# Kernel tuning notes

Measured on AMD Instinct MI355X. Metric: run time of the kernel, lower is better.

## Reference

```python
import jax, jax.numpy as jnp
import numpy as np

B, N, C = 2, 2048, 1024
H = 16
D = C // H
HID = 4 * C
EPS = 1e-5


def layernorm(x, g, b):
    mu = jnp.mean(x, axis=-1, keepdims=True)
    var = jnp.var(x, axis=-1, keepdims=True)
    return (x - mu) * jax.lax.rsqrt(var + EPS) * g + b


def setup_inputs() -> dict:
    key = jax.random.key(0)
    ks = jax.random.split(key, 8)
    s = lambda fan_in: 1.0 / np.sqrt(fan_in)
    return {
        "x": jax.random.normal(ks[0], (B, N, C), dtype=jnp.float32),
        "ln1_g": jnp.ones((C,), jnp.float32),
        "ln1_b": jnp.zeros((C,), jnp.float32),
        "w_qkv": jax.random.normal(ks[1], (C, 3 * C), jnp.float32) * s(C),
        "w_proj": jax.random.normal(ks[2], (C, C), jnp.float32) * s(C),
        "b_proj": jnp.zeros((C,), jnp.float32),
        "ln2_g": jnp.ones((C,), jnp.float32),
        "ln2_b": jnp.zeros((C,), jnp.float32),
        "w_fc1": jax.random.normal(ks[3], (C, HID), jnp.float32) * s(C),
        "b_fc1": jnp.zeros((HID,), jnp.float32),
        "w_fc2": jax.random.normal(ks[4], (HID, C), jnp.float32) * s(HID),
        "b_fc2": jnp.zeros((C,), jnp.float32),
        "metadata": 0,
        "thw_shape": 2048,
    }


def reference(x, ln1_g, ln1_b, w_qkv, w_proj, b_proj, ln2_g, ln2_b,
              w_fc1, b_fc1, w_fc2, b_fc2, metadata, thw_shape):
    scale = 1.0 / np.sqrt(D)
    # --- attention branch (pre-norm) ---
    xn = layernorm(x, ln1_g, ln1_b)
    qkv = (xn @ w_qkv).reshape(B, N, 3, H, D)
    q = jnp.transpose(qkv[:, :, 0], (0, 2, 1, 3))  # [B,H,N,D]
    k = jnp.transpose(qkv[:, :, 1], (0, 2, 1, 3))
    v = jnp.transpose(qkv[:, :, 2], (0, 2, 1, 3))
    attn = jax.nn.softmax(jnp.einsum('bhnd,bhmd->bhnm', q, k) * scale, axis=-1)
    o = jnp.einsum('bhnm,bhmd->bhnd', attn, v)
    o = jnp.transpose(o, (0, 2, 1, 3)).reshape(B, N, C)
    x = x + (o @ w_proj + b_proj)
    # --- MLP branch (pre-norm) ---
    xn2 = layernorm(x, ln2_g, ln2_b)
    h = jax.nn.gelu(xn2 @ w_fc1 + b_fc1, approximate=False)  # torch GELU = exact erf
    x = x + (h @ w_fc2 + b_fc2)
    return x
```

## Files before the change

### kernel.cpp

```cpp
#include <hip/hip_runtime.h>

#define B_   2
#define N_   2048
#define C_   1024
#define H_   16
#define D_   64
#define HID_ 4096
#define M_   (B_ * N_)

typedef __attribute__((ext_vector_type(8))) short bf16x8;
typedef __attribute__((ext_vector_type(4))) float f32x4;

__device__ __forceinline__ unsigned short f2bf(float f) {
  unsigned int u = __builtin_bit_cast(unsigned int, f);
  u += 0x7fffu + ((u >> 16) & 1u);
  return (unsigned short)(u >> 16);
}

__device__ __forceinline__ unsigned int cvtpk(float a, float b) {
  unsigned int r;
  asm("v_cvt_pk_bf16_f32 %0, %1, %2" : "=v"(r) : "v"(a), "v"(b));
  return r;
}

__device__ __forceinline__ float exp2a(float x) {
  float r;
  asm("v_exp_f32 %0, %1" : "=v"(r) : "v"(x));
  return r;
}

__device__ __forceinline__ void gl2lds16(const void* g, void* l) {
  __builtin_amdgcn_global_load_lds(
      (const __attribute__((address_space(1))) unsigned int*)g,
      (__attribute__((address_space(3))) unsigned int*)l, 16, 0, 0);
}

#define LOG2E 1.44269504088896f

__global__ __launch_bounds__(256) void ln_kernel(const float* __restrict__ x,
                                                 const float* __restrict__ g,
                                                 const float* __restrict__ bta,
                                                 unsigned short* __restrict__ out) {
  int row  = blockIdx.x * 4 + (threadIdx.x >> 6);
  int lane = threadIdx.x & 63;
  const float* xr = x + (size_t)row * C_;
  float4 v[4];
  float s1 = 0.f, s2 = 0.f;
#pragma unroll
  for (int j = 0; j < 4; j++) {
    v[j] = *(const float4*)(xr + j * 256 + lane * 4);
    s1 += v[j].x + v[j].y + v[j].z + v[j].w;
    s2 += v[j].x * v[j].x + v[j].y * v[j].y + v[j].z * v[j].z + v[j].w * v[j].w;
  }
#pragma unroll
  for (int m = 1; m < 64; m <<= 1) { s1 += __shfl_xor(s1, m); s2 += __shfl_xor(s2, m); }
  float mu  = s1 * (1.0f / C_);
  float var = s2 * (1.0f / C_) - mu * mu;
  float rs  = rsqrtf(var + 1e-5f);
#pragma unroll
  for (int j = 0; j < 4; j++) {
    const float4 gv = *(const float4*)(g + j * 256 + lane * 4);
    const float4 bv = *(const float4*)(bta + j * 256 + lane * 4);
    ushort4 o;
    o.x = f2bf((v[j].x - mu) * rs * gv.x + bv.x);
    o.y = f2bf((v[j].y - mu) * rs * gv.y + bv.y);
    o.z = f2bf((v[j].z - mu) * rs * gv.z + bv.z);
    o.w = f2bf((v[j].w - mu) * rs * gv.w + bv.w);
    *(ushort4*)(out + (size_t)row * C_ + j * 256 + lane * 4) = o;
  }
}

__global__ __launch_bounds__(256) void wtrans_all(
    const float* __restrict__ w0, const float* __restrict__ w1,
    const float* __restrict__ w2, const float* __restrict__ w3,
    unsigned short* __restrict__ o0, unsigned short* __restrict__ o1,
    unsigned short* __restrict__ o2, unsigned short* __restrict__ o3) {
  int id = blockIdx.x;
  const float* W; unsigned short* Wt; int K, N, rel;
  if (id < 3072)      { W = w0; Wt = o0; K = 1024; N = 3072; rel = id; }
  else if (id < 4096) { W = w1; Wt = o1; K = 1024; N = 1024; rel = id - 3072; }
  else if (id < 8192) { W = w2; Wt = o2; K = 1024; N = 4096; rel = id - 4096; }
  else                { W = w3; Wt = o3; K = 4096; N = 1024; rel = id - 8192; }
  int nx = N >> 5;
  int n0 = (rel % nx) * 32, k0 = (rel / nx) * 32;
  __shared__ float t[32][33];
  int tx = threadIdx.x, ty = threadIdx.y;
#pragma unroll
  for (int j = 0; j < 4; j++)
    t[ty + j * 8][tx] = W[(size_t)(k0 + ty + j * 8) * N + n0 + tx];
  __syncthreads();
#pragma unroll
  for (int j = 0; j < 4; j++)
    Wt[(size_t)(n0 + ty + j * 8) * K + k0 + tx] = f2bf(t[tx][ty + j * 8]);
}

__global__ __launch_bounds__(256) void gemm_db_kernel(
    const unsigned short* __restrict__ A,
    const unsigned short* __restrict__ Wt,
    const float* __restrict__ bias,
    const float* __restrict__ resid,
    float* __restrict__ outf,
    int M, int N, int K) {
  __shared__ __align__(16) short As[2][128][64];
  __shared__ __align__(16) short Bs[2][64][64];
  int tid = threadIdx.x;
  int w = tid >> 6, lane = tid & 63, r = lane & 15, quad = lane >> 4;
  int rowbase = w * 32;

  int nwg = gridDim.x * gridDim.y;
  int lin = blockIdx.y * gridDim.x + blockIdx.x;
  int cpx = nwg >> 3;
  lin = (lin & 7) * cpx + (lin >> 3);
  int bx = lin % gridDim.x, by = lin / gridDim.x;
  int bM = by * 128, bN = bx * 64;

  int srow   = (w << 3) + (lane >> 3);
  int schunk = (lane & 7) ^ ((lane >> 3) & 7);
  const unsigned short* aP = A  + (size_t)(bM + srow) * K + schunk * 8;
  const unsigned short* bP = Wt + (size_t)(bN + srow) * K + schunk * 8;

  int pc0 = (quad ^ (r & 7)) * 8;

  f32x4 acc[2][4];
#pragma unroll
  for (int i = 0; i < 2; i++)
#pragma unroll
    for (int j = 0; j < 4; j++) acc[i][j] = f32x4{0.f, 0.f, 0.f, 0.f};

#define STAGE_DB(kt, b)                                                       \
  do {                                                                        \
    int k0_ = (kt) * 64;                                                      \
    _Pragma("unroll") for (int p = 0; p < 4; p++)                             \
      gl2lds16(aP + (size_t)(p * 32) * K + k0_, &As[b][p * 32 + (w << 3)][0]);\
    _Pragma("unroll") for (int p = 0; p < 2; p++)                             \
      gl2lds16(bP + (size_t)(p * 32) * K + k0_, &Bs[b][p * 32 + (w << 3)][0]);\
  } while (0)

  const int nk = K >> 6;
  STAGE_DB(0, 0);
  __syncthreads();

  for (int kt = 0; kt < nk; kt++) {
    const int cb = kt & 1;
    if (kt + 1 < nk) STAGE_DB(kt + 1, cb ^ 1);
#pragma unroll
    for (int kh = 0; kh < 2; kh++) {
      int pc = pc0 ^ (kh * 32);
      bf16x8 af[2], bfr[4];
#pragma unroll
      for (int mt = 0; mt < 2; mt++)
        af[mt] = *(const bf16x8*)&As[cb][rowbase + mt * 16 + r][pc];
#pragma unroll
      for (int nt = 0; nt < 4; nt++)
        bfr[nt] = *(const bf16x8*)&Bs[cb][nt * 16 + r][pc];
#pragma unroll
      for (int mt = 0; mt < 2; mt++)
#pragma unroll
        for (int nt = 0; nt < 4; nt++)
          acc[mt][nt] = __builtin_amdgcn_mfma_f32_16x16x32_bf16(af[mt], bfr[nt], acc[mt][nt], 0, 0, 0);
    }
    __syncthreads();
  }

#pragma unroll
  for (int mt = 0; mt < 2; mt++) {
#pragma unroll
    for (int nt = 0; nt < 4; nt++) {
#pragma unroll
      for (int i = 0; i < 4; i++) {
        int gm = bM + rowbase + mt * 16 + quad * 4 + i;
        int gn = bN + nt * 16 + r;
        outf[(size_t)gm * N + gn] = acc[mt][nt][i] + bias[gn] + resid[(size_t)gm * N + gn];
      }
    }
  }
#undef STAGE_DB
}

template <int MODE>
__global__ __launch_bounds__(512, 2) void gemm256_kernel(
    const unsigned short* __restrict__ A,
    const unsigned short* __restrict__ Wt,
    const float* __restrict__ bias,
    unsigned short* __restrict__ outb0,
    unsigned short* __restrict__ outb1,
    unsigned short* __restrict__ outb2,
    int M, int N, int K) {
  __shared__ __align__(16) short As[2][256][64];
  __shared__ __align__(16) short Bs[2][256][64];
  const int tid = threadIdx.x;
  const int w = tid >> 6, lane = tid & 63, r = lane & 15, quad = lane >> 4;
  const int wr = w >> 2, wc = w & 3;

  int nwg = gridDim.x * gridDim.y;
  int lin = blockIdx.y * gridDim.x + blockIdx.x;
  int cpx = nwg >> 3;
  lin = (lin & 7) * cpx + (lin >> 3);
  const int bN = (lin % gridDim.x) * 256, bM = (lin / gridDim.x) * 256;

  const int srow   = (w << 3) + (lane >> 3);
  const int schunk = (lane & 7) ^ ((lane >> 3) & 7);
  const unsigned short* aSrc = A  + (size_t)(bM + srow) * K + schunk * 8;
  const unsigned short* bSrc = Wt + (size_t)(bN + srow) * K + schunk * 8;
  const int wrow = w << 3;

  const int ntiles = K >> 6;
  const int tmask  = ntiles - 1;

#define STAGE_H(t, h)                                                            \
  do {                                                                           \
    int b_ = (t) & 1, tt_ = (t) & tmask;                                         \
    if ((h) < 2) {                                                               \
      const unsigned short* p_ = aSrc + (size_t)((h) * 128) * K + tt_ * 64;      \
      gl2lds16(p_, &As[b_][(h) * 128 + wrow][0]);                                \
      gl2lds16(p_ + (size_t)64 * K, &As[b_][(h) * 128 + 64 + wrow][0]);          \
    } else {                                                                     \
      const unsigned short* p_ = bSrc + (size_t)(((h) - 2) * 128) * K + tt_ * 64;\
      gl2lds16(p_, &Bs[b_][((h) - 2) * 128 + wrow][0]);                          \
      gl2lds16(p_ + (size_t)64 * K, &Bs[b_][((h) - 2) * 128 + 64 + wrow][0]);    \
    }                                                                            \
  } while (0)

  f32x4 acc[8][4];
#pragma unroll
  for (int i = 0; i < 8; i++)
#pragma unroll
    for (int j = 0; j < 4; j++) acc[i][j] = f32x4{0.f, 0.f, 0.f, 0.f};

  bf16x8 af[4][2];
  bf16x8 bfr[4][2];

#define RD_A(b, msub)                                                            \
  {                                                                              \
    _Pragma("unroll") for (int mt_ = 0; mt_ < 4; mt_++)                          \
      _Pragma("unroll") for (int ks_ = 0; ks_ < 2; ks_++)                        \
        af[mt_][ks_] = *(const bf16x8*)&As[b][wr * 128 + (msub) * 64 + mt_ * 16 + r] \
                                          [((ks_ * 4 + quad) ^ (r & 7)) * 8];    \
  }
#define RD_B(b, nh)                                                              \
  {                                                                              \
    _Pragma("unroll") for (int nt_ = 0; nt_ < 2; nt_++)                          \
      _Pragma("unroll") for (int ks_ = 0; ks_ < 2; ks_++)                        \
        bfr[(nh) * 2 + nt_][ks_] =                                               \
            *(const bf16x8*)&Bs[b][wc * 64 + (nh) * 32 + nt_ * 16 + r]           \
                               [((ks_ * 4 + quad) ^ (r & 7)) * 8];               \
  }
#define MM_Q(msub, nh)                                                           \
  {                                                                              \
    _Pragma("unroll") for (int mt_ = 0; mt_ < 4; mt_++)                          \
      _Pragma("unroll") for (int nt_ = 0; nt_ < 2; nt_++)                        \
        _Pragma("unroll") for (int ks_ = 0; ks_ < 2; ks_++)                      \
          acc[(msub) * 4 + mt_][(nh) * 2 + nt_] =                                \
              __builtin_amdgcn_mfma_f32_16x16x32_bf16(                           \
                  af[mt_][ks_], bfr[(nh) * 2 + nt_][ks_],                        \
                  acc[(msub) * 4 + mt_][(nh) * 2 + nt_], 0, 0, 0);               \
  }

#define BARRIER() asm volatile("s_barrier" ::: "memory")
#define WAITL()   asm volatile("s_waitcnt lgkmcnt(0)" ::: "memory")
#define WAITV6()  asm volatile("s_waitcnt vmcnt(6)" ::: "memory")
#define PRIO1()   __builtin_amdgcn_s_setprio(1)
#define PRIO0()   __builtin_amdgcn_s_setprio(0)

  STAGE_H(0, 0); STAGE_H(0, 1); STAGE_H(0, 2); STAGE_H(0, 3);
  STAGE_H(1, 2); STAGE_H(1, 3); STAGE_H(1, 0);
  WAITV6();
  BARRIER();

  const int niter = ntiles >> 1;
  for (int i = 0; i < niter; i++) {
    const int tc = 2 * i;
    RD_A(0, 0); RD_B(0, 0);
    STAGE_H(tc + 1, 1);
    BARRIER(); WAITL();
    PRIO1(); MM_Q(0, 0); PRIO0();
    BARRIER();
    RD_B(0, 1);
    BARRIER(); WAITL();
    PRIO1(); MM_Q(0, 1); PRIO0();
    BARRIER();
    RD_A(0, 1);
    STAGE_H(tc + 2, 2);
    BARRIER(); WAITL();
    PRIO1(); MM_Q(1, 1); PRIO0();
    BARRIER();
    STAGE_H(tc + 2, 3); STAGE_H(tc + 2, 0);
    BARRIER(); WAITL();
    PRIO1(); MM_Q(1, 0); PRIO0();
    WAITV6();
    BARRIER();
    RD_A(1, 0); RD_B(1, 0);
    STAGE_H(tc + 2, 1);
    BARRIER(); WAITL();
    PRIO1(); MM_Q(0, 0); PRIO0();
    BARRIER();
    RD_B(1, 1);
    BARRIER(); WAITL();
    PRIO1(); MM_Q(0, 1); PRIO0();
    BARRIER();
    RD_A(1, 1);
    STAGE_H(tc + 3, 2);
    BARRIER(); WAITL();
    PRIO1(); MM_Q(1, 1); PRIO0();
    BARRIER();
    STAGE_H(tc + 3, 3); STAGE_H(tc + 3, 0);
    BARRIER(); WAITL();
    PRIO1(); MM_Q(1, 0); PRIO0();
    WAITV6();
    BARRIER();
  }

#pragma unroll
  for (int m = 0; m < 8; m++) {
#pragma unroll
    for (int n = 0; n < 4; n++) {
      int gm0 = bM + wr * 128 + m * 16 + quad * 4;
      int gn  = bN + wc * 64 + n * 16 + r;
      if (MODE == 0) {
        int s = gn >> 10, c = gn & 1023;
        int hh = c >> 6, d = c & 63;
        int b = gm0 >> 11, n0 = gm0 & 2047;
        if (s == 2) {
          unsigned int p0 = cvtpk(acc[m][n][0], acc[m][n][1]);
          unsigned int p1 = cvtpk(acc[m][n][2], acc[m][n][3]);
          *(uint2*)(outb2 + ((size_t)(b * H_ + hh) * D_ + d) * N_ + n0) = uint2{p0, p1};
        } else {
          unsigned short* dst = (s == 0) ? outb0 : outb1;
          float sc = (s == 0) ? 0.125f * LOG2E : 1.0f;
#pragma unroll
          for (int i2 = 0; i2 < 4; i2++) {
            size_t di = ((size_t)(b * H_ + hh) * N_ + n0 + i2) * D_ + d;
            dst[di] = f2bf(acc[m][n][i2] * sc);
          }
        }
      } else {
#pragma unroll
        for (int i2 = 0; i2 < 4; i2++) {
          float t = acc[m][n][i2] + bias[gn];
          float gl = 0.5f * t * (1.0f + erff(t * 0.70710678118f));
          outb0[(size_t)(gm0 + i2) * N + gn] = f2bf(gl);
        }
      }
    }
  }
#undef STAGE_H
#undef RD_A
#undef RD_B
#undef MM_Q
#undef BARRIER
#undef WAITL
#undef WAITV6
#undef PRIO1
#undef PRIO0
}

__global__ __launch_bounds__(512, 2) void attn_kernel(const unsigned short* __restrict__ qb,
                                                      const unsigned short* __restrict__ kb,
                                                      const unsigned short* __restrict__ vtb,
                                                      unsigned short* __restrict__ ob) {
  __shared__ __align__(16) short Ks[2][128][64];
  __shared__ __align__(16) short Vts[2][64][128];
  __shared__ __align__(16) short Pl[8 * 16 * 128];
  int tid = threadIdx.x;
  int w = tid >> 6, lane = tid & 63, r = lane & 15, quad = lane >> 4;
  int bh = blockIdx.x & 31, qt = blockIdx.x >> 5;
  const unsigned short* qh  = qb  + (size_t)bh * N_ * D_;
  const unsigned short* kh  = kb  + (size_t)bh * N_ * D_;
  const unsigned short* vth = vtb + (size_t)bh * D_ * N_;
  int swz = r & 7;

  bf16x8 qf[2][2];
#pragma unroll
  for (int mt = 0; mt < 2; mt++)
#pragma unroll
    for (int ks = 0; ks < 2; ks++)
      qf[mt][ks] = *(const bf16x8*)(qh + (size_t)(qt * 256 + w * 32 + mt * 16 + r) * D_ + ks * 32 + quad * 8);

  float mst[2] = {-1e30f, -1e30f}, lst[2] = {0.f, 0.f};
  f32x4 oacc[2][4];
#pragma unroll
  for (int mt = 0; mt < 2; mt++)
#pragma unroll
    for (int nt = 0; nt < 4; nt++) oacc[mt][nt] = f32x4{0.f, 0.f, 0.f, 0.f};

  const unsigned short* kBase = kh + (size_t)(tid >> 3) * D_ + ((tid & 7) ^ ((tid >> 3) & 7)) * 8;
  const unsigned short* vBase = vth + (size_t)(tid >> 4) * N_ + ((tid & 15) ^ ((tid >> 4) & 7)) * 8;

  short* Plw = &Pl[0] + w * 2048;

  gl2lds16(kBase,                        &Ks[0][(w << 3)][0]);
  gl2lds16(kBase + (size_t)64 * D_,      &Ks[0][64 + (w << 3)][0]);
  gl2lds16(vBase,                        &Vts[0][(w << 2)][0]);
  gl2lds16(vBase + (size_t)32 * N_,      &Vts[0][32 + (w << 2)][0]);
  __syncthreads();

  for (int t = 0; t < 16; t++) {
    const int cur = t & 1;
    if (t < 15) {
      const int nb = cur ^ 1;
      gl2lds16(kBase + (size_t)(t + 1) * 128 * D_,                  &Ks[nb][(w << 3)][0]);
      gl2lds16(kBase + (size_t)((t + 1) * 128 + 64) * D_,           &Ks[nb][64 + (w << 3)][0]);
      gl2lds16(vBase + (size_t)(t + 1) * 128,                       &Vts[nb][(w << 2)][0]);
      gl2lds16(vBase + (size_t)(t + 1) * 128 + (size_t)32 * N_,     &Vts[nb][32 + (w << 2)][0]);
    }

    f32x4 sacc[2][8];
#pragma unroll
    for (int mt = 0; mt < 2; mt++)
#pragma unroll
      for (int nt = 0; nt < 8; nt++) sacc[mt][nt] = f32x4{0.f, 0.f, 0.f, 0.f};
#pragma unroll
    for (int ks = 0; ks < 2; ks++) {
#pragma unroll
      for (int nt = 0; nt < 8; nt++) {
        bf16x8 kfr = *(const bf16x8*)&Ks[cur][nt * 16 + r][((ks * 4 + quad) ^ swz) * 8];
#pragma unroll
        for (int mt = 0; mt < 2; mt++)
          sacc[mt][nt] = __builtin_amdgcn_mfma_f32_16x16x32_bf16(kfr, qf[mt][ks], sacc[mt][nt], 0, 0, 0);
      }
    }

    bf16x8 vfr[4][4];
#pragma unroll
    for (int ks = 0; ks < 4; ks++)
#pragma unroll
      for (int nt2 = 0; nt2 < 4; nt2++)
        vfr[ks][nt2] = *(const bf16x8*)&Vts[cur][nt2 * 16 + r][((ks * 4 + quad) ^ swz) * 8];

#pragma unroll
    for (int mt = 0; mt < 2; mt++) {
      float tm = -1e30f;
#pragma unroll
      for (int nt = 0; nt < 8; nt++)
#pragma unroll
        for (int i = 0; i < 4; i++) tm = fmaxf(tm, sacc[mt][nt][i]);
      tm = fmaxf(tm, __shfl_xor(tm, 16));
      tm = fmaxf(tm, __shfl_xor(tm, 32));
      if (__ballot(tm > mst[mt] + 8.0f)) {
        float mnew = fmaxf(mst[mt], tm);
        float alpha = exp2a(mst[mt] - mnew);
        mst[mt] = mnew;
        lst[mt] *= alpha;
#pragma unroll
        for (int i = 0; i < 4; i++) {
          float av = __shfl(alpha, (lane & 48) | (quad * 4 + i));
#pragma unroll
          for (int nt2 = 0; nt2 < 4; nt2++) oacc[mt][nt2][i] *= av;
        }
      }
      float m = mst[mt];
      float rs = 0.f;
#pragma unroll
      for (int nt = 0; nt < 8; nt++)
#pragma unroll
        for (int i = 0; i < 4; i++) {
          float p = exp2a(sacc[mt][nt][i] - m);
          sacc[mt][nt][i] = p;
          rs += p;
        }
      rs += __shfl_xor(rs, 16);
      rs += __shfl_xor(rs, 32);
      lst[mt] += rs;
    }

#pragma unroll
    for (int mt = 0; mt < 2; mt++) {
#pragma unroll
      for (int nt = 0; nt < 8; nt++) {
        uint2 pw;
        pw.x = cvtpk(sacc[mt][nt][0], sacc[mt][nt][1]);
        pw.y = cvtpk(sacc[mt][nt][2], sacc[mt][nt][3]);
        *(uint2*)&Plw[r * 128 + (((nt * 2 + (quad >> 1)) ^ swz) * 8) + (quad & 1) * 4] = pw;
      }
      asm volatile("" ::: "memory");
#pragma unroll
      for (int ks = 0; ks < 4; ks++) {
        bf16x8 pfr = *(const bf16x8*)&Plw[r * 128 + ((ks * 4 + quad) ^ swz) * 8];
#pragma unroll
        for (int nt2 = 0; nt2 < 4; nt2++)
          oacc[mt][nt2] = __builtin_amdgcn_mfma_f32_16x16x32_bf16(pfr, vfr[ks][nt2], oacc[mt][nt2], 0, 0, 0);
      }
      asm volatile("" ::: "memory");
    }

    __syncthreads();
  }

  int bb = bh >> 4, hh = bh & 15;
#pragma unroll
  for (int mt = 0; mt < 2; mt++) {
#pragma unroll
    for (int i = 0; i < 4; i++) {
      float li = __shfl(lst[mt], (lane & 48) | (quad * 4 + i));
      float inv = 1.0f / li;
      int row = qt * 256 + w * 32 + mt * 16 + quad * 4 + i;
#pragma unroll
      for (int nt2 = 0; nt2 < 4; nt2++) {
        int d = nt2 * 16 + r;
        ob[((size_t)bb * N_ + row) * C_ + hh * D_ + d] = f2bf(oacc[mt][nt2][i] * inv);
      }
    }
  }
}

extern "C" void kernel_launch(void* const* d_in, const int* in_sizes, int n_in,
                              void* d_out, int out_size, void* d_ws, size_t ws_size,
                              hipStream_t stream) {
  const float* x     = (const float*)d_in[0];
  const float* ln1g  = (const float*)d_in[1];
  const float* ln1b  = (const float*)d_in[2];
  const float* wqkv  = (const float*)d_in[3];
  const float* wproj = (const float*)d_in[4];
  const float* bproj = (const float*)d_in[5];
  const float* ln2g  = (const float*)d_in[6];
  const float* ln2b  = (const float*)d_in[7];
  const float* wfc1  = (const float*)d_in[8];
  const float* bfc1  = (const float*)d_in[9];
  const float* wfc2  = (const float*)d_in[10];
  const float* bfc2  = (const float*)d_in[11];
  float* out = (float*)d_out;

  const size_t MB = 1u << 20;
  if (ws_size < 88 * MB) return;
  char* w = (char*)d_ws;
  unsigned short* xn    = (unsigned short*)(w + 0 * MB);
  unsigned short* qbuf  = (unsigned short*)(w + 8 * MB);
  unsigned short* kbuf  = (unsigned short*)(w + 16 * MB);
  unsigned short* hbuf  = (unsigned short*)(w + 0 * MB);
  unsigned short* obuf  = (unsigned short*)(w + 32 * MB);
  float*          x2    = (float*)         (w + 40 * MB);
  unsigned short* xn2   = (unsigned short*)(w + 56 * MB);
  unsigned short* vtb   = (unsigned short*)(w + 56 * MB);
  unsigned short* wqkvt = (unsigned short*)(w + 64 * MB);
  unsigned short* wprjt = (unsigned short*)(w + 70 * MB);
  unsigned short* wfc1t = (unsigned short*)(w + 72 * MB);
  unsigned short* wfc2t = (unsigned short*)(w + 80 * MB);

  ln_kernel<<<M_ / 4, 256, 0, stream>>>(x, ln1g, ln1b, xn);
  wtrans_all<<<12288, dim3(32, 8), 0, stream>>>(wqkv, wproj, wfc1, wfc2,
                                                wqkvt, wprjt, wfc1t, wfc2t);

  gemm256_kernel<0><<<dim3(3 * C_ / 256, M_ / 256), 512, 0, stream>>>(
      xn, wqkvt, nullptr, qbuf, kbuf, vtb, M_, 3 * C_, C_);
  attn_kernel<<<B_ * H_ * (N_ / 256), 512, 0, stream>>>(qbuf, kbuf, vtb, obuf);
  gemm_db_kernel<<<dim3(C_ / 64, M_ / 128), 256, 0, stream>>>(
      obuf, wprjt, bproj, x, x2, M_, C_, C_);
  ln_kernel<<<M_ / 4, 256, 0, stream>>>(x2, ln2g, ln2b, xn2);
  gemm256_kernel<2><<<dim3(HID_ / 256, M_ / 256), 512, 0, stream>>>(
      xn2, wfc1t, bfc1, hbuf, nullptr, nullptr, M_, HID_, C_);
  gemm_db_kernel<<<dim3(C_ / 64, M_ / 128), 256, 0, stream>>>(
      hbuf, wfc2t, bfc2, x2, out, M_, C_, HID_);
}
```

Baseline: 353.0 us.

## Replace 256x256 pipelined GEMM with templated 128x128 double-buffered GEMM

Removes the hand-scheduled 256x256 tile GEMM (with priority hints, partial waits and interleaved staging) and generalizes the simpler double-buffered GEMM with a template over epilogue mode and N tile width. The QKV and FC1 GEMMs now use 128x128 tiles with 256 threads, while the projection and FC2 GEMMs keep 128x64. This yields more, smaller workgroups and simpler code, at the cost of less operand reuse per tile and losing the fine-grained load/compute overlap.

```diff
diff --git a/kernel.cpp b/kernel.cpp
--- a/kernel.cpp
+++ b/kernel.cpp
@@ -94,25 +94,31 @@
     Wt[(size_t)(n0 + ty + j * 8) * K + k0 + tx] = f2bf(t[tx][ty + j * 8]);
 }
 
+template <int MODE, int BN>
 __global__ __launch_bounds__(256) void gemm_db_kernel(
     const unsigned short* __restrict__ A,
     const unsigned short* __restrict__ Wt,
     const float* __restrict__ bias,
     const float* __restrict__ resid,
     float* __restrict__ outf,
+    unsigned short* __restrict__ outb0,
+    unsigned short* __restrict__ outb1,
+    unsigned short* __restrict__ outb2,
     int M, int N, int K) {
+  constexpr int MT = (BN == 128) ? 4 : 2;
   __shared__ __align__(16) short As[2][128][64];
-  __shared__ __align__(16) short Bs[2][64][64];
+  __shared__ __align__(16) short Bs[2][BN][64];
   int tid = threadIdx.x;
   int w = tid >> 6, lane = tid & 63, r = lane & 15, quad = lane >> 4;
-  int rowbase = w * 32;
+  int rowbase = (BN == 128) ? (w >> 1) * 64 : w * 32;
+  int colbase = (BN == 128) ? (w & 1) * 64 : 0;
 
   int nwg = gridDim.x * gridDim.y;
   int lin = blockIdx.y * gridDim.x + blockIdx.x;
   int cpx = nwg >> 3;
   lin = (lin & 7) * cpx + (lin >> 3);
   int bx = lin % gridDim.x, by = lin / gridDim.x;
-  int bM = by * 128, bN = bx * 64;
+  int bM = by * 128, bN = bx * BN;
 
   int srow   = (w << 3) + (lane >> 3);
   int schunk = (lane & 7) ^ ((lane >> 3) & 7);
@@ -121,9 +127,9 @@
 
   int pc0 = (quad ^ (r & 7)) * 8;
 
-  f32x4 acc[2][4];
-#pragma unroll
-  for (int i = 0; i < 2; i++)
+  f32x4 acc[MT][4];
+#pragma unroll
+  for (int i = 0; i < MT; i++)
 #pragma unroll
     for (int j = 0; j < 4; j++) acc[i][j] = f32x4{0.f, 0.f, 0.f, 0.f};
 
@@ -132,7 +138,7 @@
     int k0_ = (kt) * 64;                                                      \
     _Pragma("unroll") for (int p = 0; p < 4; p++)                             \
       gl2lds16(aP + (size_t)(p * 32) * K + k0_, &As[b][p * 32 + (w << 3)][0]);\
-    _Pragma("unroll") for (int p = 0; p < 2; p++)                             \
+    _Pragma("unroll") for (int p = 0; p < BN / 32; p++)                       \
       gl2lds16(bP + (size_t)(p * 32) * K + k0_, &Bs[b][p * 32 + (w << 3)][0]);\
   } while (0)
 
@@ -146,15 +152,15 @@
 #pragma unroll
     for (int kh = 0; kh < 2; kh++) {
       int pc = pc0 ^ (kh * 32);
-      bf16x8 af[2], bfr[4];
-#pragma unroll
-      for (int mt = 0; mt < 2; mt++)
+      bf16x8 af[MT], bfr[4];
+#pragma unroll
+      for (int mt = 0; mt < MT; mt++)
         af[mt] = *(const bf16x8*)&As[cb][rowbase + mt * 16 + r][pc];
 #pragma unroll
       for (int nt = 0; nt < 4; nt++)
-        bfr[nt] = *(const bf16x8*)&Bs[cb][nt * 16 + r][pc];
-#pragma unroll
-      for (int mt = 0; mt < 2; mt++)
+        bfr[nt] = *(const bf16x8*)&Bs[cb][colbase + nt * 16 + r][pc];
+#pragma unroll
+      for (int mt = 0; mt < MT; mt++)
 #pragma unroll
         for (int nt = 0; nt < 4; nt++)
           acc[mt][nt] = __builtin_amdgcn_mfma_f32_16x16x32_bf16(af[mt], bfr[nt], acc[mt][nt], 0, 0, 0);
@@ -163,166 +169,18 @@
   }
 
 #pragma unroll
-  for (int mt = 0; mt < 2; mt++) {
+  for (int mt = 0; mt < MT; mt++) {
 #pragma unroll
     for (int nt = 0; nt < 4; nt++) {
-#pragma unroll
-      for (int i = 0; i < 4; i++) {
-        int gm = bM + rowbase + mt * 16 + quad * 4 + i;
-        int gn = bN + nt * 16 + r;
-        outf[(size_t)gm * N + gn] = acc[mt][nt][i] + bias[gn] + resid[(size_t)gm * N + gn];
-      }
-    }
-  }
-#undef STAGE_DB
-}
-
-template <int MODE>
-__global__ __launch_bounds__(512, 2) void gemm256_kernel(
-    const unsigned short* __restrict__ A,
-    const unsigned short* __restrict__ Wt,
-    const float* __restrict__ bias,
-    unsigned short* __restrict__ outb0,
-    unsigned short* __restrict__ outb1,
-    unsigned short* __restrict__ outb2,
-    int M, int N, int K) {
-  __shared__ __align__(16) short As[2][256][64];
-  __shared__ __align__(16) short Bs[2][256][64];
-  const int tid = threadIdx.x;
-  const int w = tid >> 6, lane = tid & 63, r = lane & 15, quad = lane >> 4;
-  const int wr = w >> 2, wc = w & 3;
-
-  int nwg = gridDim.x * gridDim.y;
-  int lin = blockIdx.y * gridDim.x + blockIdx.x;
-  int cpx = nwg >> 3;
-  lin = (lin & 7) * cpx + (lin >> 3);
-  const int bN = (lin % gridDim.x) * 256, bM = (lin / gridDim.x) * 256;
-
-  const int srow   = (w << 3) + (lane >> 3);
-  const int schunk = (lane & 7) ^ ((lane >> 3) & 7);
-  const unsigned short* aSrc = A  + (size_t)(bM + srow) * K + schunk * 8;
-  const unsigned short* bSrc = Wt + (size_t)(bN + srow) * K + schunk * 8;
-  const int wrow = w << 3;
-
-  const int ntiles = K >> 6;
-  const int tmask  = ntiles - 1;
-
-#define STAGE_H(t, h)                                                            \
-  do {                                                                           \
-    int b_ = (t) & 1, tt_ = (t) & tmask;                                         \
-    if ((h) < 2) {                                                               \
-      const unsigned short* p_ = aSrc + (size_t)((h) * 128) * K + tt_ * 64;      \
-      gl2lds16(p_, &As[b_][(h) * 128 + wrow][0]);                                \
-      gl2lds16(p_ + (size_t)64 * K, &As[b_][(h) * 128 + 64 + wrow][0]);          \
-    } else {                                                                     \
-      const unsigned short* p_ = bSrc + (size_t)(((h) - 2) * 128) * K + tt_ * 64;\
-      gl2lds16(p_, &Bs[b_][((h) - 2) * 128 + wrow][0]);                          \
-      gl2lds16(p_ + (size_t)64 * K, &Bs[b_][((h) - 2) * 128 + 64 + wrow][0]);    \
-    }                                                                            \
-  } while (0)
-
-  f32x4 acc[8][4];
-#pragma unroll
-  for (int i = 0; i < 8; i++)
-#pragma unroll
-    for (int j = 0; j < 4; j++) acc[i][j] = f32x4{0.f, 0.f, 0.f, 0.f};
-
-  bf16x8 af[4][2];
-  bf16x8 bfr[4][2];
-
-#define RD_A(b, msub)                                                            \
-  {                                                                              \
-    _Pragma("unroll") for (int mt_ = 0; mt_ < 4; mt_++)                          \
-      _Pragma("unroll") for (int ks_ = 0; ks_ < 2; ks_++)                        \
-        af[mt_][ks_] = *(const bf16x8*)&As[b][wr * 128 + (msub) * 64 + mt_ * 16 + r] \
-                                          [((ks_ * 4 + quad) ^ (r & 7)) * 8];    \
-  }
-#define RD_B(b, nh)                                                              \
-  {                                                                              \
-    _Pragma("unroll") for (int nt_ = 0; nt_ < 2; nt_++)                          \
-      _Pragma("unroll") for (int ks_ = 0; ks_ < 2; ks_++)                        \
-        bfr[(nh) * 2 + nt_][ks_] =                                               \
-            *(const bf16x8*)&Bs[b][wc * 64 + (nh) * 32 + nt_ * 16 + r]           \
-                               [((ks_ * 4 + quad) ^ (r & 7)) * 8];               \
-  }
-#define MM_Q(msub, nh)                                                           \
-  {                                                                              \
-    _Pragma("unroll") for (int mt_ = 0; mt_ < 4; mt_++)                          \
-      _Pragma("unroll") for (int nt_ = 0; nt_ < 2; nt_++)                        \
-        _Pragma("unroll") for (int ks_ = 0; ks_ < 2; ks_++)                      \
-          acc[(msub) * 4 + mt_][(nh) * 2 + nt_] =                                \
-              __builtin_amdgcn_mfma_f32_16x16x32_bf16(                           \
-                  af[mt_][ks_], bfr[(nh) * 2 + nt_][ks_],                        \
-                  acc[(msub) * 4 + mt_][(nh) * 2 + nt_], 0, 0, 0);               \
-  }
-
-#define BARRIER() asm volatile("s_barrier" ::: "memory")
-#define WAITL()   asm volatile("s_waitcnt lgkmcnt(0)" ::: "memory")
-#define WAITV6()  asm volatile("s_waitcnt vmcnt(6)" ::: "memory")
-#define PRIO1()   __builtin_amdgcn_s_setprio(1)
-#define PRIO0()   __builtin_amdgcn_s_setprio(0)
-
-  STAGE_H(0, 0); STAGE_H(0, 1); STAGE_H(0, 2); STAGE_H(0, 3);
-  STAGE_H(1, 2); STAGE_H(1, 3); STAGE_H(1, 0);
-  WAITV6();
-  BARRIER();
-
-  const int niter = ntiles >> 1;
-  for (int i = 0; i < niter; i++) {
-    const int tc = 2 * i;
-    RD_A(0, 0); RD_B(0, 0);
-    STAGE_H(tc + 1, 1);
-    BARRIER(); WAITL();
-    PRIO1(); MM_Q(0, 0); PRIO0();
-    BARRIER();
-    RD_B(0, 1);
-    BARRIER(); WAITL();
-    PRIO1(); MM_Q(0, 1); PRIO0();
-    BARRIER();
-    RD_A(0, 1);
-    STAGE_H(tc + 2, 2);
-    BARRIER(); WAITL();
-    PRIO1(); MM_Q(1, 1); PRIO0();
-    BARRIER();
-    STAGE_H(tc + 2, 3); STAGE_H(tc + 2, 0);
-    BARRIER(); WAITL();
-    PRIO1(); MM_Q(1, 0); PRIO0();
-    WAITV6();
-    BARRIER();
-    RD_A(1, 0); RD_B(1, 0);
-    STAGE_H(tc + 2, 1);
-    BARRIER(); WAITL();
-    PRIO1(); MM_Q(0, 0); PRIO0();
-    BARRIER();
-    RD_B(1, 1);
-    BARRIER(); WAITL();
-    PRIO1(); MM_Q(0, 1); PRIO0();
-    BARRIER();
-    RD_A(1, 1);
-    STAGE_H(tc + 3, 2);
-    BARRIER(); WAITL();
-    PRIO1(); MM_Q(1, 1); PRIO0();
-    BARRIER();
-    STAGE_H(tc + 3, 3); STAGE_H(tc + 3, 0);
-    BARRIER(); WAITL();
-    PRIO1(); MM_Q(1, 0); PRIO0();
-    WAITV6();
-    BARRIER();
-  }
-
-#pragma unroll
-  for (int m = 0; m < 8; m++) {
-#pragma unroll
-    for (int n = 0; n < 4; n++) {
-      int gm0 = bM + wr * 128 + m * 16 + quad * 4;
-      int gn  = bN + wc * 64 + n * 16 + r;
+      int gm0 = bM + rowbase + mt * 16 + quad * 4;
+      int gn  = bN + colbase + nt * 16 + r;
       if (MODE == 0) {
         int s = gn >> 10, c = gn & 1023;
         int hh = c >> 6, d = c & 63;
         int b = gm0 >> 11, n0 = gm0 & 2047;
         if (s == 2) {
-          unsigned int p0 = cvtpk(acc[m][n][0], acc[m][n][1]);
-          unsigned int p1 = cvtpk(acc[m][n][2], acc[m][n][3]);
+          unsigned int p0 = cvtpk(acc[mt][nt][0], acc[mt][nt][1]);
+          unsigned int p1 = cvtpk(acc[mt][nt][2], acc[mt][nt][3]);
           *(uint2*)(outb2 + ((size_t)(b * H_ + hh) * D_ + d) * N_ + n0) = uint2{p0, p1};
         } else {
           unsigned short* dst = (s == 0) ? outb0 : outb1;
@@ -330,28 +188,26 @@
 #pragma unroll
           for (int i2 = 0; i2 < 4; i2++) {
             size_t di = ((size_t)(b * H_ + hh) * N_ + n0 + i2) * D_ + d;
-            dst[di] = f2bf(acc[m][n][i2] * sc);
+            dst[di] = f2bf(acc[mt][nt][i2] * sc);
           }
         }
+      } else if (MODE == 1) {
+#pragma unroll
+        for (int i2 = 0; i2 < 4; i2++) {
+          int gm = gm0 + i2;
+          outf[(size_t)gm * N + gn] = acc[mt][nt][i2] + bias[gn] + resid[(size_t)gm * N + gn];
+        }
       } else {
 #pragma unroll
         for (int i2 = 0; i2 < 4; i2++) {
-          float t = acc[m][n][i2] + bias[gn];
+          float t = acc[mt][nt][i2] + bias[gn];
           float gl = 0.5f * t * (1.0f + erff(t * 0.70710678118f));
           outb0[(size_t)(gm0 + i2) * N + gn] = f2bf(gl);
         }
       }
     }
   }
-#undef STAGE_H
-#undef RD_A
-#undef RD_B
-#undef MM_Q
-#undef BARRIER
-#undef WAITL
-#undef WAITV6
-#undef PRIO1
-#undef PRIO0
+#undef STAGE_DB
 }
 
 __global__ __launch_bounds__(512, 2) void attn_kernel(const unsigned short* __restrict__ qb,
@@ -540,14 +396,14 @@
   wtrans_all<<<12288, dim3(32, 8), 0, stream>>>(wqkv, wproj, wfc1, wfc2,
                                                 wqkvt, wprjt, wfc1t, wfc2t);
 
-  gemm256_kernel<0><<<dim3(3 * C_ / 256, M_ / 256), 512, 0, stream>>>(
-      xn, wqkvt, nullptr, qbuf, kbuf, vtb, M_, 3 * C_, C_);
+  gemm_db_kernel<0, 128><<<dim3(3 * C_ / 128, M_ / 128), 256, 0, stream>>>(
+      xn, wqkvt, nullptr, nullptr, nullptr, qbuf, kbuf, vtb, M_, 3 * C_, C_);
   attn_kernel<<<B_ * H_ * (N_ / 256), 512, 0, stream>>>(qbuf, kbuf, vtb, obuf);
-  gemm_db_kernel<<<dim3(C_ / 64, M_ / 128), 256, 0, stream>>>(
-      obuf, wprjt, bproj, x, x2, M_, C_, C_);
+  gemm_db_kernel<1, 64><<<dim3(C_ / 64, M_ / 128), 256, 0, stream>>>(
+      obuf, wprjt, bproj, x, x2, nullptr, nullptr, nullptr, M_, C_, C_);
   ln_kernel<<<M_ / 4, 256, 0, stream>>>(x2, ln2g, ln2b, xn2);
-  gemm256_kernel<2><<<dim3(HID_ / 256, M_ / 256), 512, 0, stream>>>(
-      xn2, wfc1t, bfc1, hbuf, nullptr, nullptr, M_, HID_, C_);
-  gemm_db_kernel<<<dim3(C_ / 64, M_ / 128), 256, 0, stream>>>(
-      hbuf, wfc2t, bfc2, x2, out, M_, C_, HID_);
-}
+  gemm_db_kernel<2, 128><<<dim3(HID_ / 128, M_ / 128), 256, 0, stream>>>(
+      xn2, wfc1t, bfc1, nullptr, nullptr, hbuf, nullptr, nullptr, M_, HID_, C_);
+  gemm_db_kernel<1, 64><<<dim3(C_ / 64, M_ / 128), 256, 0, stream>>>(
+      hbuf, wfc2t, bfc2, x2, out, nullptr, nullptr, nullptr, M_, C_, HID_);
+}
```

Result: no change. 355.0 us (+0.6%).
